# Kernel tuning notes

Measured on AMD Instinct MI355X. Metric: run time of the kernel, lower is better.

The kernel has to match this reference:

```python
import jax, jax.numpy as jnp
import numpy as np
from jax import lax

B, S_ENC, T, M = 32, 200, 400, 80
E2 = 512          # 2 * encoder_hidden_dim
H = 1024          # decoder_hidden_dim
IN0 = M + E2      # LSTM layer-0 input size


def setup_inputs() -> dict:
    key = jax.random.key(0)
    ks = jax.random.split(key, 16)
    s = 1.0 / np.sqrt(H)  # pytorch LSTM-style uniform scale ~ 1/sqrt(H)
    def rn(k, shape, scale):
        return jax.random.normal(k, shape, jnp.float32) * scale
    return {
        "encoder_outputs": rn(ks[0], (B, S_ENC, E2), 1.0),
        "audio_targets": rn(ks[1], (B, T, M), 1.0),
        "Wih0": rn(ks[2], (4 * H, IN0), s),
        "Whh0": rn(ks[3], (4 * H, H), s),
        "bih0": rn(ks[4], (4 * H,), s),
        "bhh0": rn(ks[5], (4 * H,), s),
        "Wih1": rn(ks[6], (4 * H, H), s),
        "Whh1": rn(ks[7], (4 * H, H), s),
        "bih1": rn(ks[8], (4 * H,), s),
        "bhh1": rn(ks[9], (4 * H,), s),
        "Wa": rn(ks[10], (1, H + E2), s),
        "ba": rn(ks[11], (1,), s),
        "Wfc": rn(ks[12], (M, H), s),
        "bfc": rn(ks[13], (M,), s),
        "audio_lengths": jax.random.randint(ks[14], (B,), 1, T + 1, dtype=jnp.int32),
    }


def _lstm_cell(x, h, c, Wih, Whh, b):
    # PyTorch gate order: i, f, g, o
    g = x @ Wih.T + h @ Whh.T + b
    i, f, gg, o = jnp.split(g, 4, axis=-1)
    c2 = jax.nn.sigmoid(f) * c + jax.nn.sigmoid(i) * jnp.tanh(gg)
    h2 = jax.nn.sigmoid(o) * jnp.tanh(c2)
    return h2, c2


def reference(encoder_outputs, audio_targets, Wih0, Whh0, bih0, bhh0,
              Wih1, Whh1, bih1, bhh1, Wa, ba, Wfc, bfc, audio_lengths):
    del audio_lengths  # unused in the original forward
    Hd = Whh0.shape[1]
    b0 = bih0 + bhh0
    b1 = bih1 + bhh1
    # tanh(concat(h, enc)) == concat(tanh(h), tanh(enc)) -> precompute enc part of the score once
    wa_h = Wa[0, :Hd]                 # [H]
    wa_e = Wa[0, Hd:]                 # [E2]
    enc_score = jnp.einsum('bse,e->bs', jnp.tanh(encoder_outputs), wa_e)  # [B,S]

    def step(carry, x_t):
        h0, c0, h1, c1 = carry
        score = enc_score + (jnp.tanh(h1) @ wa_h)[:, None] + ba[0]        # [B,S]
        w = jax.nn.softmax(score, axis=1)
        ctx = jnp.einsum('bs,bse->be', w, encoder_outputs)                # [B,E2]
        inp = jnp.concatenate([x_t, ctx], axis=-1)                        # [B,IN0]
        h0, c0 = _lstm_cell(inp, h0, c0, Wih0, Whh0, b0)
        h1, c1 = _lstm_cell(h0, h1, c1, Wih1, Whh1, b1)
        pred = h1 @ Wfc.T + bfc                                            # [B,M]
        return (h0, c0, h1, c1), pred

    bsz = encoder_outputs.shape[0]
    z = jnp.zeros((bsz, Hd), encoder_outputs.dtype)
    # t = 0: hidden is None -> context is mean over encoder steps, zero initial state
    ctx0 = encoder_outputs.mean(axis=1)
    inp0 = jnp.concatenate([audio_targets[:, 0, :], ctx0], axis=-1)
    h0, c0 = _lstm_cell(inp0, z, z, Wih0, Whh0, b0)
    h1, c1 = _lstm_cell(h0, z, z, Wih1, Whh1, b1)
    pred0 = h1 @ Wfc.T + bfc

    xs = jnp.swapaxes(audio_targets, 0, 1)[1:]                             # [T-1,B,M]
    _, preds = lax.scan(step, (h0, c0, h1, c1), xs)                        # [T-1,B,M]
    out = jnp.concatenate([pred0[:, None, :], jnp.swapaxes(preds, 0, 1)], axis=1)
    return out                                                             # [B,T,M]
```

## Files before the change

### kernel.cpp

```cpp
#include <hip/hip_runtime.h>
#include <hip/hip_cooperative_groups.h>

namespace cg = cooperative_groups;

#define BBAT 32
#define SE 200
#define TT 400
#define MM 80
#define EE 512
#define HH 1024
#define IN0 592
#define KS 608
#define NSC 19
#define W0S 1640
#define W1STR 1032
#define NBLK 256
#define NTHR 512

#define NGRP 16
#define GSZ  16
#define BSLOTS 272

typedef __attribute__((ext_vector_type(4))) float f32x4;
typedef __attribute__((ext_vector_type(8))) short s16x8;
typedef unsigned long long u64;

#define OFF_W0    0
#define OFF_W1I   52480
#define OFF_W1H   85504
#define OFF_GRED  118528
#define OFF_C0    151296
#define OFF_C1    151808
#define OFF_BS    152320
#define LDS_TOTAL 152448

#define WS_XSTAT 0
#define WS_H0B   15564800
#define WS_H1B   15696896
#define WS_H1F   15828992
#define WS_ESC   16222208
#define WS_CST   16247808
#define WS_BAR   16378880

__device__ __forceinline__ float sigmf(float x){ return 1.0f/(1.0f+expf(-x)); }

__device__ __forceinline__ unsigned short f2bf(float v){
  unsigned int u = __float_as_uint(v);
  u += 0x7fffu + ((u >> 16) & 1u);
  return (unsigned short)(u >> 16);
}

__device__ __forceinline__ void st64a(void* p, u64 v){
  __hip_atomic_store((u64*)p, v, __ATOMIC_RELAXED, __HIP_MEMORY_SCOPE_AGENT);
}
__device__ __forceinline__ u64 ld64a(const void* p){
  return __hip_atomic_load((const u64*)p, __ATOMIC_RELAXED, __HIP_MEMORY_SCOPE_AGENT);
}
__device__ __forceinline__ float2 ld2f(const float* p){
  u64 q = ld64a(p);
  float2 r; r.x = __uint_as_float((unsigned)q); r.y = __uint_as_float((unsigned)(q >> 32));
  return r;
}
__device__ __forceinline__ u64 pk2f(float a, float b){
  return ((u64)__float_as_uint(b) << 32) | (u64)__float_as_uint(a);
}

#define LD4C(d0,d1,d2,d3,p0,p1,p2,p3) \
  asm volatile("global_load_dwordx4 %0, %4, off sc0 sc1\n\t" \
               "global_load_dwordx4 %1, %5, off sc0 sc1\n\t" \
               "global_load_dwordx4 %2, %6, off sc0 sc1\n\t" \
               "global_load_dwordx4 %3, %7, off sc0 sc1" \
               : "=&v"(d0), "=&v"(d1), "=&v"(d2), "=&v"(d3) \
               : "v"(p0), "v"(p1), "v"(p2), "v"(p3))

#define WAIT16(a0,a1,a2,a3,b0,b1,b2,b3,c0,c1,c2,c3,d0,d1,d2,d3) \
  asm volatile("s_waitcnt vmcnt(0)" \
    : "+v"(a0),"+v"(a1),"+v"(a2),"+v"(a3), \
      "+v"(b0),"+v"(b1),"+v"(b2),"+v"(b3), \
      "+v"(c0),"+v"(c1),"+v"(c2),"+v"(c3), \
      "+v"(d0),"+v"(d1),"+v"(d2),"+v"(d3))

__device__ __forceinline__ void gbar_arrive(unsigned* slots){
  __builtin_amdgcn_s_waitcnt(0);
  __syncthreads();
  if (threadIdx.x == 0){
    const unsigned g = blockIdx.x >> 4;
    unsigned prev = __hip_atomic_fetch_add(slots + g*16, 1u, __ATOMIC_RELAXED, __HIP_MEMORY_SCOPE_AGENT);
    if (prev == (unsigned)(GSZ-1))
      __hip_atomic_fetch_add(slots + NGRP*16, 1u, __ATOMIC_RELAXED, __HIP_MEMORY_SCOPE_AGENT);
  }
}
__device__ __forceinline__ void gbar_wait(unsigned* slots){
  if (threadIdx.x == 0){
    while (__hip_atomic_load(slots + NGRP*16, __ATOMIC_RELAXED, __HIP_MEMORY_SCOPE_AGENT) < (unsigned)NGRP)
      __builtin_amdgcn_s_sleep(1);
  }
  __syncthreads();
}

__device__ __forceinline__ float bsum(float v, float* red){
  #pragma unroll
  for (int o = 32; o; o >>= 1) v += __shfl_down(v, o);
  __syncthreads();
  if ((threadIdx.x & 63) == 0) red[threadIdx.x >> 6] = v;
  __syncthreads();
  float s = 0.f;
  #pragma unroll
  for (int w2 = 0; w2 < 8; ++w2) s += red[w2];
  return s;
}
__device__ __forceinline__ float bmax(float v, float* red){
  #pragma unroll
  for (int o = 32; o; o >>= 1) v = fmaxf(v, __shfl_down(v, o));
  __syncthreads();
  if ((threadIdx.x & 63) == 0) red[threadIdx.x >> 6] = v;
  __syncthreads();
  float s = -3.4e38f;
  #pragma unroll
  for (int w2 = 0; w2 < 8; ++w2) s = fmaxf(s, red[w2]);
  return s;
}

#define MFMA16(a,b,c) __builtin_amdgcn_mfma_f32_16x16x32_bf16((a),(b),(c),0,0,0)

__device__ __forceinline__ void mfma_static(const unsigned short* __restrict__ xs,
    const unsigned short* __restrict__ W0, int w, int row, int kg,
    f32x4& acc0, f32x4& acc1)
{
  for (int c = w; c < NSC; c += 8) {
    const int off = (c << 5) + (kg << 3);
    s16x8 a0 = *(const s16x8*)(xs + (size_t)row*KS + off);
    s16x8 a1 = *(const s16x8*)(xs + (size_t)(row+16)*KS + off);
    s16x8 bw = *(const s16x8*)(W0 + row*W0S + off);
    acc0 = MFMA16(a0, bw, acc0);
    acc1 = MFMA16(a1, bw, acc1);
  }
}

__global__ void __launch_bounds__(NTHR, 1) decoder_kernel(
    const float* __restrict__ enc, const float* __restrict__ audio,
    const float* __restrict__ Wih0, const float* __restrict__ Whh0,
    const float* __restrict__ bih0, const float* __restrict__ bhh0,
    const float* __restrict__ Wih1, const float* __restrict__ Whh1,
    const float* __restrict__ bih1, const float* __restrict__ bhh1,
    const float* __restrict__ Wa, const float* __restrict__ ba,
    const float* __restrict__ Wfc, const float* __restrict__ bfc,
    float* __restrict__ out, float* __restrict__ ws)
{
  cg::grid_group grid = cg::this_grid();
  extern __shared__ char lds[];
  unsigned short* W0  = (unsigned short*)(lds + OFF_W0);
  unsigned short* W1I = (unsigned short*)(lds + OFF_W1I);
  unsigned short* W1H = (unsigned short*)(lds + OFF_W1H);
  float* Gred = (float*)(lds + OFF_GRED);
  float* c0l  = (float*)(lds + OFF_C0);
  float* c1l  = (float*)(lds + OFF_C1);
  float* b0s  = (float*)(lds + OFF_BS);
  float* b1s  = b0s + 16;
  float* smw  = Gred;
  float* red  = Gred + 256;

  const int blk = blockIdx.x, tid = threadIdx.x;
  const int j = blk;
  const int w = tid >> 6, lane = tid & 63;
  const int row = lane & 15, kg = lane >> 4;
  const int cblk = j >> 3;
  const int colw = (j & 7) << 2;
  const int eg = tid & 3, ep = (tid >> 2) & 3, eb = tid >> 4;

  unsigned short* xstat = (unsigned short*)((char*)ws + WS_XSTAT);
  unsigned short* h0b   = (unsigned short*)((char*)ws + WS_H0B);
  unsigned short* h1b   = (unsigned short*)((char*)ws + WS_H1B);
  float* h1f  = (float*)((char*)ws + WS_H1F);
  float* esc  = (float*)((char*)ws + WS_ESC);
  float* cm   = (float*)((char*)ws + WS_CST);
  float* cs   = cm + BBAT*EE;
  unsigned* bars = (unsigned*)((char*)ws + WS_BAR);

  for (int i = tid; i < 16*W0S; i += NTHR) {
    int r = i / W0S, k = i - r*W0S;
    int n = (r & 3)*HH + 4*j + (r >> 2);
    float v = 0.f;
    if (k < IN0) v = Wih0[(size_t)n*IN0 + k];
    else if (k >= KS && k < KS + HH) v = Whh0[(size_t)n*HH + (k - KS)];
    W0[i] = f2bf(v);
  }
  for (int i = tid; i < 16*W1STR; i += NTHR) {
    int r = i / W1STR, k = i - r*W1STR;
    int n = (r & 3)*HH + 4*j + (r >> 2);
    W1I[i] = (k < HH) ? f2bf(Wih1[(size_t)n*HH + k]) : (unsigned short)0;
    W1H[i] = (k < HH) ? f2bf(Whh1[(size_t)n*HH + k]) : (unsigned short)0;
  }
  if (tid < 16) {
    int p = tid >> 2, g = tid & 3, n = g*HH + 4*j + p;
    b0s[tid] = bih0[n] + bhh0[n];
    b1s[tid] = bih1[n] + bhh1[n];
  }
  if (tid < 128) { c0l[tid] = 0.f; c1l[tid] = 0.f; }
  for (int i = blk*NTHR + tid; i < 2*BBAT*HH; i += NBLK*NTHR) { h0b[i] = 0; h1b[i] = 0; }
  for (int i = blk*NTHR + tid; i < 3*BBAT*HH; i += NBLK*NTHR) h1f[i] = 0.f;
  for (int i = blk*NTHR + tid; i < (TT+2)*BSLOTS; i += NBLK*NTHR) bars[i] = 0u;
  for (int r2 = blk; r2 < BBAT*SE; r2 += NBLK) {
    float pp = tanhf(enc[(size_t)r2*EE + tid]) * Wa[HH + tid];
    pp = bsum(pp, red);
    if (tid == 0) esc[r2] = pp;
  }
  grid.sync();

  if (blk < BBAT) {
    const int b = blk;
    float sc = (tid < SE) ? esc[b*SE + tid] : -3.4e38f;
    float mx = bmax(sc, red);
    float ex = (tid < SE) ? expf(sc - mx) : 0.f;
    float den = bsum(ex, red);
    if (tid < SE) smw[tid] = ex / den;
    __syncthreads();
    const int e = tid;
    float as = 0.f, am = 0.f;
    for (int s = 0; s < SE; ++s) {
      float v = enc[((size_t)b*SE + s)*EE + e];
      as = fmaf(smw[s], v, as);
      am += v;
    }
    cm[b*EE + e] = am * (1.0f/(float)SE);
    cs[b*EE + e] = as;
  }
  grid.sync();

  for (int t2 = blk; t2 < TT; t2 += NBLK) {
    const float* cx = (t2 == 0) ? cm : cs;
    for (int b = 0; b < BBAT; ++b) {
      for (int k = tid; k < KS; k += NTHR) {
        float v;
        if (k < MM)        v = audio[((size_t)b*TT + t2)*MM + k];
        else if (k < IN0)  v = cx[b*EE + (k - MM)];
        else               v = 0.f;
        xstat[((size_t)t2*BBAT + b)*KS + k] = f2bf(v);
      }
    }
  }
  grid.sync();

  const f32x4 z4 = {0.f,0.f,0.f,0.f};
  f32x4 accP0 = z4, accP1 = z4;

  mfma_static(xstat, W0, w, row, kg, accP0, accP1);
  {
    float* gw = Gred + (w << 10) + row;
    #pragma unroll
    for (int v = 0; v < 4; ++v) {
      gw[(((kg<<2)+v)    << 4)] = accP0[v];
      gw[(((kg<<2)+v+16) << 4)] = accP1[v];
    }
    __syncthreads();
    float s0 = 0.f;
    #pragma unroll
    for (int w8 = 0; w8 < 8; ++w8) s0 += Gred[(w8 << 10) + tid];
    float ga = s0;
    float gb = __shfl_xor(s0, 1);
    float gc = __shfl_xor(s0, 2);
    float gd = __shfl_xor(gb, 2);
    if (eg == 0) {
      f32x4 bi = *(const f32x4*)(b0s + (ep << 2));
      float gi = ga + bi[0], gf = gb + bi[1], gg = gc + bi[2], go = gd + bi[3];
      float cn = sigmf(gi) * tanhf(gg);
      c0l[ep*32 + eb] = cn;
      float hn = sigmf(go) * tanhf(cn);
      float hB = __shfl_xor(hn, 4);
      float hC = __shfl_xor(hn, 8);
      float hD = __shfl_xor(hB, 8);
      if ((tid & 15) == 0) {
        u64 hp = (u64)f2bf(hn) | ((u64)f2bf(hB) << 16) | ((u64)f2bf(hC) << 32) | ((u64)f2bf(hD) << 48);
        st64a(h0b + (cblk << 10) + (eb << 5) + colw, hp);
      }
    }
  }
  gbar_arrive(bars);
  accP0 = z4; accP1 = z4;
  mfma_static(xstat + (size_t)BBAT*KS, W0, w, row, kg, accP0, accP1);
  gbar_wait(bars);

  for (int t = 0; t < TT; ++t) {
    const unsigned short* h0R = h0b + (t&1)*BBAT*HH;
    const unsigned short* h1R = h1b + ((t&1)^1)*BBAT*HH;
    unsigned short* h1W = h1b + (t&1)*BBAT*HH;
    unsigned short* h0Wn = h0b + ((t+1)&1)*BBAT*HH;
    float* h1fW = h1f + (size_t)(t % 3)*BBAT*HH;

    s16x8 A0h[4], A1h[4], A0g[4], A1g[4];
    {
      const unsigned short* ph0a  = h0R + (row << 5) + (kg << 3);
      const unsigned short* ph0b_ = h0R + ((row+16) << 5) + (kg << 3);
      const unsigned short* ph1a  = h1R + (row << 5) + (kg << 3);
      const unsigned short* ph1b_ = h1R + ((row+16) << 5) + (kg << 3);
      const int o0 = (w << 10), o1 = ((w+8) << 10), o2_ = ((w+16) << 10), o3 = ((w+24) << 10);
      LD4C(A0h[0],A0h[1],A0h[2],A0h[3], ph0a+o0, ph0a+o1, ph0a+o2_, ph0a+o3);
      LD4C(A1h[0],A1h[1],A1h[2],A1h[3], ph0b_+o0, ph0b_+o1, ph0b_+o2_, ph0b_+o3);
      LD4C(A0g[0],A0g[1],A0g[2],A0g[3], ph1a+o0, ph1a+o1, ph1a+o2_, ph1a+o3);
      LD4C(A1g[0],A1g[1],A1g[2],A1g[3], ph1b_+o0, ph1b_+o1, ph1b_+o2_, ph1b_+o3);
      WAIT16(A0h[0],A0h[1],A0h[2],A0h[3], A1h[0],A1h[1],A1h[2],A1h[3],
             A0g[0],A0g[1],A0g[2],A0g[3], A1g[0],A1g[1],A1g[2],A1g[3]);
    }
    f32x4 q0 = z4, q1 = z4;
    #pragma unroll
    for (int i = 0; i < 4; ++i) {
      const int off = ((w + (i << 3)) << 5) + (kg << 3);
      s16x8 b1 = *(const s16x8*)(W1I + row*W1STR + off);
      q0 = MFMA16(A0h[i], b1, q0);
      q1 = MFMA16(A1h[i], b1, q1);
      s16x8 b0 = *(const s16x8*)(W0 + row*W0S + KS + off);
      accP0 = MFMA16(A0h[i], b0, accP0);
      accP1 = MFMA16(A1h[i], b0, accP1);
      s16x8 b2 = *(const s16x8*)(W1H + row*W1STR + off);
      q0 = MFMA16(A0g[i], b2, q0);
      q1 = MFMA16(A1g[i], b2, q1);
    }
    {
      float* gw = Gred + (w << 10) + row;
      #pragma unroll
      for (int v = 0; v < 4; ++v) {
        gw[(((kg<<2)+v)    << 4)]       = accP0[v];
        gw[(((kg<<2)+v+16) << 4)]       = accP1[v];
        gw[512 + (((kg<<2)+v)    << 4)] = q0[v];
        gw[512 + (((kg<<2)+v+16) << 4)] = q1[v];
      }
      __syncthreads();
      float s0 = 0.f, s1 = 0.f;
      #pragma unroll
      for (int w8 = 0; w8 < 8; ++w8) {
        s0 += Gred[(w8 << 10) + tid];
        s1 += Gred[(w8 << 10) + 512 + tid];
      }
      float a0g_ = s0;
      float b0g_ = __shfl_xor(s0, 1);
      float c0g_ = __shfl_xor(s0, 2);
      float d0g_ = __shfl_xor(b0g_, 2);
      float a1g_ = s1;
      float b1g_ = __shfl_xor(s1, 1);
      float c1g_ = __shfl_xor(s1, 2);
      float d1g_ = __shfl_xor(b1g_, 2);
      if (eg == 0) {
        f32x4 bi1 = *(const f32x4*)(b1s + (ep << 2));
        float gi = a1g_ + bi1[0], gf = b1g_ + bi1[1], gg = c1g_ + bi1[2], go = d1g_ + bi1[3];
        float cn1 = sigmf(gf) * c1l[ep*32 + eb] + sigmf(gi) * tanhf(gg);
        c1l[ep*32 + eb] = cn1;
        float hn1 = sigmf(go) * tanhf(cn1);
        f32x4 bi0 = *(const f32x4*)(b0s + (ep << 2));
        float fi = a0g_ + bi0[0], ff = b0g_ + bi0[1], fg = c0g_ + bi0[2], fo = d0g_ + bi0[3];
        float cn0 = sigmf(ff) * c0l[ep*32 + eb] + sigmf(fi) * tanhf(fg);
        c0l[ep*32 + eb] = cn0;
        float hn0 = sigmf(fo) * tanhf(cn0);
        float h1B = __shfl_xor(hn1, 4);
        float h1C = __shfl_xor(hn1, 8);
        float h1D = __shfl_xor(h1B, 8);
        float h0B = __shfl_xor(hn0, 4);
        float h0C = __shfl_xor(hn0, 8);
        float h0D = __shfl_xor(h0B, 8);
        if ((tid & 15) == 0) {
          u64 hp1 = (u64)f2bf(hn1) | ((u64)f2bf(h1B) << 16) | ((u64)f2bf(h1C) << 32) | ((u64)f2bf(h1D) << 48);
          st64a(h1W + (cblk << 10) + (eb << 5) + colw, hp1);
          st64a(h1fW + (size_t)eb*HH + 4*j,     pk2f(hn1, h1B));
          st64a(h1fW + (size_t)eb*HH + 4*j + 2, pk2f(h1C, h1D));
          u64 hp0 = (u64)f2bf(hn0) | ((u64)f2bf(h0B) << 16) | ((u64)f2bf(h0C) << 32) | ((u64)f2bf(h0D) << 48);
          st64a(h0Wn + (cblk << 10) + (eb << 5) + colw, hp0);
        }
      }
    }
    gbar_arrive(bars + (size_t)(t+1)*BSLOTS);

    if (t >= 1) {
      const float* h1fF = h1f + (size_t)((t-1) % 3)*BBAT*HH;
      for (int u = w; u < 10; u += 8) {
        int idx = j*10 + u;
        int b = idx / MM, m = idx - b*MM;
        float pp = 0.f;
        #pragma unroll
        for (int cq = 0; cq < 4; ++cq) {
          float2 h0v = ld2f(h1fF + (size_t)b*HH + cq*256 + lane*4);
          float2 h1v = ld2f(h1fF + (size_t)b*HH + cq*256 + lane*4 + 2);
          float4 wv = *(const float4*)(Wfc + (size_t)m*HH + cq*256 + lane*4);
          pp = fmaf(h0v.x,wv.x, fmaf(h0v.y,wv.y, fmaf(h1v.x,wv.z, fmaf(h1v.y,wv.w, pp))));
        }
        #pragma unroll
        for (int o2 = 32; o2; o2 >>= 1) pp += __shfl_down(pp, o2);
        if (lane == 0) out[((size_t)b*TT + (t-1))*MM + m] = pp + bfc[m];
      }
    }
    accP0 = z4; accP1 = z4;
    if (t + 2 < TT)
      mfma_static(xstat + (size_t)(t+2)*BBAT*KS, W0, w, row, kg, accP0, accP1);
    gbar_wait(bars + (size_t)(t+1)*BSLOTS);
  }

  {
    const float* h1fL = h1f + (size_t)((TT-1) % 3)*BBAT*HH;
    for (int u = w; u < 10; u += 8) {
      int idx = j*10 + u;
      int b = idx / MM, m = idx - b*MM;
      float pp = 0.f;
      #pragma unroll
      for (int cq = 0; cq < 4; ++cq) {
        float2 h0v = ld2f(h1fL + (size_t)b*HH + cq*256 + lane*4);
        float2 h1v = ld2f(h1fL + (size_t)b*HH + cq*256 + lane*4 + 2);
        float4 wv = *(const float4*)(Wfc + (size_t)m*HH + cq*256 + lane*4);
        pp = fmaf(h0v.x,wv.x, fmaf(h0v.y,wv.y, fmaf(h1v.x,wv.z, fmaf(h1v.y,wv.w, pp))));
      }
      #pragma unroll
      for (int o2 = 32; o2; o2 >>= 1) pp += __shfl_down(pp, o2);
      if (lane == 0) out[((size_t)b*TT + (TT-1))*MM + m] = pp + bfc[m];
    }
  }
}

extern "C" void kernel_launch(void* const* d_in, const int* in_sizes, int n_in,
                              void* d_out, int out_size, void* d_ws, size_t ws_size,
                              hipStream_t stream) {
  const float* enc  = (const float*)d_in[0];
  const float* audio= (const float*)d_in[1];
  const float* Wih0 = (const float*)d_in[2];
  const float* Whh0 = (const float*)d_in[3];
  const float* bih0 = (const float*)d_in[4];
  const float* bhh0 = (const float*)d_in[5];
  const float* Wih1 = (const float*)d_in[6];
  const float* Whh1 = (const float*)d_in[7];
  const float* bih1 = (const float*)d_in[8];
  const float* bhh1 = (const float*)d_in[9];
  const float* Wa   = (const float*)d_in[10];
  const float* ba   = (const float*)d_in[11];
  const float* Wfc  = (const float*)d_in[12];
  const float* bfc  = (const float*)d_in[13];
  float* out = (float*)d_out;
  float* ws  = (float*)d_ws;

  (void)hipFuncSetAttribute((const void*)decoder_kernel,
                            hipFuncAttributeMaxDynamicSharedMemorySize, LDS_TOTAL);

  void* args[] = { &enc,&audio,&Wih0,&Whh0,&bih0,&bhh0,&Wih1,&Whh1,&bih1,&bhh1,
                   &Wa,&ba,&Wfc,&bfc,&out,&ws };
  hipLaunchCooperativeKernel((const void*)decoder_kernel, dim3(NBLK), dim3(NTHR),
                             args, LDS_TOTAL, stream);
}
```

Measured before the change: 3.096 ms.

## Replace grid-wide step barrier with per-column-block dataflow flags

Replaces the hierarchical grid barrier at each timestep with per-column-block arrival counters. Each wave spins only on the flags for the h0/h1 chunks it actually reads, and the final projection waits only on the last-step h1 flags. This is meant to remove the global barrier latency and let blocks proceed as soon as their dependencies are ready. The cost is more flag polling per wave and a risk of ordering or WAR hazards on the double- and triple-buffered state.

```diff
diff --git a/kernel.cpp b/kernel.cpp
--- a/kernel.cpp
+++ b/kernel.cpp
@@ -17,10 +17,6 @@
 #define NBLK 256
 #define NTHR 512
 
-#define NGRP 16
-#define GSZ  16
-#define BSLOTS 272
-
 typedef __attribute__((ext_vector_type(4))) float f32x4;
 typedef __attribute__((ext_vector_type(8))) short s16x8;
 typedef unsigned long long u64;
@@ -40,7 +36,9 @@
 #define WS_H1F   15828992
 #define WS_ESC   16222208
 #define WS_CST   16247808
-#define WS_BAR   16378880
+#define WS_FLG   16378880
+#define H1OFFU   ((TT+1)*32*4)
+#define FLGN     (2*(TT+1)*32*4)
 
 __device__ __forceinline__ float sigmf(float x){ return 1.0f/(1.0f+expf(-x)); }
 
@@ -79,24 +77,6 @@
       "+v"(b0),"+v"(b1),"+v"(b2),"+v"(b3), \
       "+v"(c0),"+v"(c1),"+v"(c2),"+v"(c3), \
       "+v"(d0),"+v"(d1),"+v"(d2),"+v"(d3))
-
-__device__ __forceinline__ void gbar_arrive(unsigned* slots){
-  __builtin_amdgcn_s_waitcnt(0);
-  __syncthreads();
-  if (threadIdx.x == 0){
-    const unsigned g = blockIdx.x >> 4;
-    unsigned prev = __hip_atomic_fetch_add(slots + g*16, 1u, __ATOMIC_RELAXED, __HIP_MEMORY_SCOPE_AGENT);
-    if (prev == (unsigned)(GSZ-1))
-      __hip_atomic_fetch_add(slots + NGRP*16, 1u, __ATOMIC_RELAXED, __HIP_MEMORY_SCOPE_AGENT);
-  }
-}
-__device__ __forceinline__ void gbar_wait(unsigned* slots){
-  if (threadIdx.x == 0){
-    while (__hip_atomic_load(slots + NGRP*16, __ATOMIC_RELAXED, __HIP_MEMORY_SCOPE_AGENT) < (unsigned)NGRP)
-      __builtin_amdgcn_s_sleep(1);
-  }
-  __syncthreads();
-}
 
 __device__ __forceinline__ float bsum(float v, float* red){
   #pragma unroll
@@ -175,7 +155,7 @@
   float* esc  = (float*)((char*)ws + WS_ESC);
   float* cm   = (float*)((char*)ws + WS_CST);
   float* cs   = cm + BBAT*EE;
-  unsigned* bars = (unsigned*)((char*)ws + WS_BAR);
+  unsigned* flg = (unsigned*)((char*)ws + WS_FLG);
 
   for (int i = tid; i < 16*W0S; i += NTHR) {
     int r = i / W0S, k = i - r*W0S;
@@ -199,7 +179,7 @@
   if (tid < 128) { c0l[tid] = 0.f; c1l[tid] = 0.f; }
   for (int i = blk*NTHR + tid; i < 2*BBAT*HH; i += NBLK*NTHR) { h0b[i] = 0; h1b[i] = 0; }
   for (int i = blk*NTHR + tid; i < 3*BBAT*HH; i += NBLK*NTHR) h1f[i] = 0.f;
-  for (int i = blk*NTHR + tid; i < (TT+2)*BSLOTS; i += NBLK*NTHR) bars[i] = 0u;
+  for (int i = blk*NTHR + tid; i < FLGN; i += NBLK*NTHR) flg[i] = 0u;
   for (int r2 = blk; r2 < BBAT*SE; r2 += NBLK) {
     float pp = tanhf(enc[(size_t)r2*EE + tid]) * Wa[HH + tid];
     pp = bsum(pp, red);
@@ -263,6 +243,7 @@
     if (eg == 0) {
       f32x4 bi = *(const f32x4*)(b0s + (ep << 2));
       float gi = ga + bi[0], gf = gb + bi[1], gg = gc + bi[2], go = gd + bi[3];
+      (void)gf;
       float cn = sigmf(gi) * tanhf(gg);
       c0l[ep*32 + eb] = cn;
       float hn = sigmf(go) * tanhf(cn);
@@ -275,10 +256,12 @@
       }
     }
   }
-  gbar_arrive(bars);
+  __builtin_amdgcn_s_waitcnt(0);
+  __syncthreads();
+  if (tid == 0)
+    __hip_atomic_fetch_add(flg + (size_t)cblk*4, 1u, __ATOMIC_RELAXED, __HIP_MEMORY_SCOPE_AGENT);
   accP0 = z4; accP1 = z4;
   mfma_static(xstat + (size_t)BBAT*KS, W0, w, row, kg, accP0, accP1);
-  gbar_wait(bars);
 
   for (int t = 0; t < TT; ++t) {
     const unsigned short* h0R = h0b + (t&1)*BBAT*HH;
@@ -286,6 +269,20 @@
     unsigned short* h1W = h1b + (t&1)*BBAT*HH;
     unsigned short* h0Wn = h0b + ((t+1)&1)*BBAT*HH;
     float* h1fW = h1f + (size_t)(t % 3)*BBAT*HH;
+
+    {
+      const int pc = w + ((lane & 3) << 3);
+      if (lane < 4) {
+        unsigned* fp = flg + ((size_t)t*32 + pc)*4;
+        while (__hip_atomic_load(fp, __ATOMIC_RELAXED, __HIP_MEMORY_SCOPE_AGENT) < 8u)
+          __builtin_amdgcn_s_sleep(1);
+      } else if (lane < 8 && t > 0) {
+        unsigned* fp = flg + H1OFFU + ((size_t)(t-1)*32 + pc)*4;
+        while (__hip_atomic_load(fp, __ATOMIC_RELAXED, __HIP_MEMORY_SCOPE_AGENT) < 8u)
+          __builtin_amdgcn_s_sleep(1);
+      }
+      asm volatile("" ::: "memory");
+    }
 
     s16x8 A0h[4], A1h[4], A0g[4], A1g[4];
     {
@@ -366,7 +363,12 @@
         }
       }
     }
-    gbar_arrive(bars + (size_t)(t+1)*BSLOTS);
+    __builtin_amdgcn_s_waitcnt(0);
+    __syncthreads();
+    if (tid == 0) {
+      __hip_atomic_fetch_add(flg + ((size_t)(t+1)*32 + cblk)*4, 1u, __ATOMIC_RELAXED, __HIP_MEMORY_SCOPE_AGENT);
+      __hip_atomic_fetch_add(flg + H1OFFU + ((size_t)t*32 + cblk)*4, 1u, __ATOMIC_RELAXED, __HIP_MEMORY_SCOPE_AGENT);
+    }
 
     if (t >= 1) {
       const float* h1fF = h1f + (size_t)((t-1) % 3)*BBAT*HH;
@@ -389,9 +391,14 @@
     accP0 = z4; accP1 = z4;
     if (t + 2 < TT)
       mfma_static(xstat + (size_t)(t+2)*BBAT*KS, W0, w, row, kg, accP0, accP1);
-    gbar_wait(bars + (size_t)(t+1)*BSLOTS);
-  }
-
+  }
+
+  if (tid < 32) {
+    unsigned* fp = flg + H1OFFU + ((size_t)(TT-1)*32 + tid)*4;
+    while (__hip_atomic_load(fp, __ATOMIC_RELAXED, __HIP_MEMORY_SCOPE_AGENT) < 8u)
+      __builtin_amdgcn_s_sleep(1);
+  }
+  __syncthreads();
   {
     const float* h1fL = h1f + (size_t)((TT-1) % 3)*BBAT*HH;
     for (int u = w; u < 10; u += 8) {
```

Result: faster. 2.847 ms (-8.1%).
